# Performance work log

Measured on AMD Instinct MI355X. Metric: run time of the kernel, lower is better.

## Reference

```python
import jax, jax.numpy as jnp
import numpy as np

B, L = 1, 2048
HID, NH, VOCAB = 1024, 12, 50257
KD, VD = 768, 1536            # key_dim = 0.75*1024, value_dim = 1.5*1024
DK, DV = KD // NH, VD // NH   # 64, 128
CONV_K = 4
EPS = 1e-5

def silu(x):
    return x * jax.nn.sigmoid(x)

def short_conv(x, w):
    # causal depthwise conv1d: x [B,T,D], w [D,K]; y[t] = sum_i w[:,i]*x[t-(K-1)+i]
    T = x.shape[1]
    K = w.shape[1]
    xp = jnp.pad(x, ((0, 0), (K - 1, 0), (0, 0)))
    y = xp[:, 0:T, :] * w[:, 0]
    for i in range(1, K):
        y = y + xp[:, i:i + T, :] * w[:, i]
    return y

def l2norm(x):
    return x * jax.lax.rsqrt(jnp.sum(x * x, -1, keepdims=True) + 1e-6)

def setup_inputs() -> dict:
    key = jax.random.key(0)
    ks = jax.random.split(key, 16)
    n = lambda k, shape, s: jax.random.normal(k, shape, jnp.float32) * s
    dt = jnp.exp(jax.random.uniform(ks[12], (NH,)) * (np.log(0.1) - np.log(0.001)) + np.log(0.001))
    dt = jnp.clip(dt, 1e-4, None)
    return {
        "hidden_states": jax.random.randint(ks[0], (B, L), 0, VOCAB),
        "emb": n(ks[1], (VOCAB, HID), 0.02),
        "Wq": n(ks[2], (KD, HID), 0.02),
        "Wk": n(ks[3], (KD, HID), 0.02),
        "Wv": n(ks[4], (VD, HID), 0.02),
        "Wg": n(ks[5], (VD, HID), 0.02),
        "wq_conv": n(ks[6], (KD, CONV_K), 0.3),
        "wk_conv": n(ks[7], (KD, CONV_K), 0.3),
        "wv_conv": n(ks[8], (VD, CONV_K), 0.3),
        "Wgk": n(ks[9], (NH, HID), 0.02),
        "Wb": n(ks[10], (NH, HID), 0.02),
        "b_b": jnp.zeros((NH,), jnp.float32),
        "A_log": jnp.log(jax.random.uniform(ks[11], (NH,), minval=1.0, maxval=16.0)),
        "dt_bias": dt + jnp.log(-jnp.expm1(-dt)),
        "g_norm_w": jnp.ones((DV,), jnp.float32),
        "Wo": n(ks[13], (HID, VD), 0.02),
        "Wlm": n(ks[14], (VOCAB, HID), 0.02),
        "b_lm": jnp.zeros((VOCAB,), jnp.float32),
    }

def reference(hidden_states, emb, Wq, Wk, Wv, Wg, wq_conv, wk_conv, wv_conv,
              Wgk, Wb, b_b, A_log, dt_bias, g_norm_w, Wo, Wlm, b_lm):
    x = emb[hidden_states]                                   # [B,L,HID]
    q = silu(short_conv(x @ Wq.T, wq_conv))                  # [B,L,KD]
    k = silu(short_conv(x @ Wk.T, wk_conv))                  # [B,L,KD]
    v = silu(short_conv(x @ Wv.T, wv_conv))                  # [B,L,VD]
    # mamba-style per-head log-decay gate
    gk = -jnp.exp(A_log) * jax.nn.softplus(x @ Wgk.T + dt_bias)  # [B,L,NH]
    beta = jax.nn.sigmoid(x @ Wb.T + b_b)                        # [B,L,NH]
    q = l2norm(q.reshape(B, L, NH, DK)) * (DK ** -0.5)
    k = l2norm(k.reshape(B, L, NH, DK))
    v = v.reshape(B, L, NH, DV)
    # time-major for the gated delta-rule recurrence
    qs = q.transpose(1, 0, 2, 3)
    ks_ = k.transpose(1, 0, 2, 3)
    vs = v.transpose(1, 0, 2, 3)
    gks = gk.transpose(1, 0, 2)
    bs = beta.transpose(1, 0, 2)
    S0 = jnp.zeros((B, NH, DK, DV), jnp.float32)

    def step(S, inp):
        q_t, k_t, v_t, g_t, b_t = inp                        # [B,NH,DK],[B,NH,DK],[B,NH,DV],[B,NH],[B,NH]
        S = S * jnp.exp(g_t)[..., None, None]                # per-head scalar decay
        v_old = jnp.einsum('bhk,bhkv->bhv', k_t, S)
        dv = (v_t - v_old) * b_t[..., None]                  # delta-rule correction
        S = S + k_t[..., None] * dv[:, :, None, :]           # rank-1 update
        o_t = jnp.einsum('bhk,bhkv->bhv', q_t, S)
        return S, o_t

    _, o = jax.lax.scan(step, S0, (qs, ks_, vs, gks, bs))    # [L,B,NH,DV]
    o = o.transpose(1, 0, 2, 3)                              # [B,L,NH,DV]
    g = (x @ Wg.T).reshape(B, L, NH, DV)
    # fused RMSNorm + swish gate: rmsnorm(o) * g * sigmoid(g)
    o = o * jax.lax.rsqrt(jnp.mean(o * o, -1, keepdims=True) + EPS) * g_norm_w
    o = o * silu(g)
    o = o.reshape(B, L, VD) @ Wo.T                           # [B,L,HID]
    return o @ Wlm.T + b_lm                                  # [B,L,VOCAB]
```

## Files before the change

kernel.cpp:

```cpp
#include <hip/hip_runtime.h>
#include <math.h>

typedef float fx4 __attribute__((ext_vector_type(4)));
typedef _Float16 hx8 __attribute__((ext_vector_type(8)));
typedef _Float16 hx4 __attribute__((ext_vector_type(4)));

#define GL16(g, l) __builtin_amdgcn_global_load_lds( \
    (const __attribute__((address_space(1))) void*)(g), \
    (__attribute__((address_space(3))) void*)(l), 16, 0, 0)

template<bool NTL>
__global__ __launch_bounds__(256)
void cvt16(const float* __restrict__ in, _Float16* __restrict__ outh, int n8)
{
  int i = blockIdx.x * 256 + threadIdx.x;
  if (i < n8){
    fx4 a, b;
    if (NTL){
      a = __builtin_nontemporal_load((const fx4*)(in + (size_t)i * 8));
      b = __builtin_nontemporal_load((const fx4*)(in + (size_t)i * 8 + 4));
    } else {
      a = *(const fx4*)(in + (size_t)i * 8);
      b = *(const fx4*)(in + (size_t)i * 8 + 4);
    }
    hx8 h;
    #pragma unroll
    for (int e = 0; e < 4; e++){ h[e] = (_Float16)a[e]; h[4+e] = (_Float16)b[e]; }
    *(hx8*)(outh + (size_t)i * 8) = h;
  }
}

__global__ __launch_bounds__(256)
void embed_k(const int* __restrict__ ids, const float* __restrict__ emb,
             float* __restrict__ x, _Float16* __restrict__ xh)
{
  int t = blockIdx.x;
  int id = ids[t];
  fx4 v = *(const fx4*)(emb + (size_t)id * 1024 + threadIdx.x * 4);
  *(fx4*)(x + (size_t)t * 1024 + threadIdx.x * 4) = v;
  hx4 h;
  #pragma unroll
  for (int e = 0; e < 4; e++) h[e] = (_Float16)v[e];
  *(hx4*)(xh + (size_t)t * 1024 + threadIdx.x * 4) = h;
}

template<int MT, int NT, int WR, int WC, bool OUT16>
__global__ __launch_bounds__(WR*WC*64, 2)
void gemm_hh(const _Float16* __restrict__ A, const _Float16* __restrict__ B,
             void* __restrict__ Cv, const float* __restrict__ bias,
             int M, int N, int K)
{
  constexpr int BM = WR*MT*16, BN = WC*NT*16;
  constexpr int T  = WR*WC*64;
  constexpr int ABYTES = BM*128, BUF = ABYTES + BN*128;
  constexpr int FA = BM*8/T, FB = BN*8/T;
  static_assert(FA + FB == 4, "vmcnt literal assumes 4 loads/thread/tile");
  __shared__ __align__(16) char smem[2*BUF];

  const int tid = threadIdx.x;
  const int lane = tid & 63, w = tid >> 6;
  const int wr = w / WC, wc = w % WC;
  const int lm = lane & 15, lg = lane >> 4;
  const int nk = K >> 6;

  const int nwgx = gridDim.x, nwg = nwgx * gridDim.y;
  int orig = blockIdx.y * nwgx + blockIdx.x;
  int logical = (orig & 7) * (nwg >> 3) + (orig >> 3);
  const int m0 = (logical % nwgx) * BM, n0 = (logical / nwgx) * BN;

  const char* gsA[FA];
  const char* gsB[FB];
  int fdA[FA], fdB[FB];
  #pragma unroll
  for (int j = 0; j < FA; j++){
    int f = tid + j*T;
    int row = f >> 3, oct = (f & 7) ^ (row & 7);
    gsA[j] = (const char*)(A + (size_t)(m0 + row) * K + oct * 8);
    fdA[j] = f * 16;
  }
  #pragma unroll
  for (int j = 0; j < FB; j++){
    int f = tid + j*T;
    int row = f >> 3, oct = (f & 7) ^ (row & 7);
    int rb = n0 + row; if (rb > N - 1) rb = N - 1;
    gsB[j] = (const char*)(B + (size_t)rb * K + oct * 8);
    fdB[j] = ABYTES + f * 16;
  }

  fx4 acc[MT][NT];
  #pragma unroll
  for (int mt = 0; mt < MT; mt++)
    #pragma unroll
    for (int nt = 0; nt < NT; nt++)
      acc[mt][nt] = (fx4){0.f, 0.f, 0.f, 0.f};

  #pragma unroll
  for (int j = 0; j < FA; j++) GL16(gsA[j], smem + fdA[j]);
  #pragma unroll
  for (int j = 0; j < FB; j++) GL16(gsB[j], smem + fdB[j]);
  if (nk > 1){
    #pragma unroll
    for (int j = 0; j < FA; j++) GL16(gsA[j] + 128, smem + BUF + fdA[j]);
    #pragma unroll
    for (int j = 0; j < FB; j++) GL16(gsB[j] + 128, smem + BUF + fdB[j]);
  }

  for (int kt = 0; kt < nk; kt++){
    if (kt + 1 < nk) asm volatile("s_waitcnt vmcnt(4)" ::: "memory");
    else             asm volatile("s_waitcnt vmcnt(0)" ::: "memory");
    asm volatile("s_barrier" ::: "memory");

    const char* bp = smem + (kt & 1) * BUF;
    #pragma unroll
    for (int s = 0; s < 2; s++){
      hx8 af[MT], bfr[NT];
      #pragma unroll
      for (int mt = 0; mt < MT; mt++){
        int row = wr*MT*16 + mt*16 + lm;
        af[mt] = *(const hx8*)(bp + row*128 + (((s*4 + lg) ^ (row & 7)) << 4));
      }
      #pragma unroll
      for (int nt = 0; nt < NT; nt++){
        int row = wc*NT*16 + nt*16 + lm;
        bfr[nt] = *(const hx8*)(bp + ABYTES + row*128 + (((s*4 + lg) ^ (row & 7)) << 4));
      }
      #pragma unroll
      for (int mt = 0; mt < MT; mt++)
        #pragma unroll
        for (int nt = 0; nt < NT; nt++)
          acc[mt][nt] = __builtin_amdgcn_mfma_f32_16x16x32_f16(af[mt], bfr[nt], acc[mt][nt], 0, 0, 0);
    }
    asm volatile("s_barrier" ::: "memory");

    if (kt + 2 < nk){
      char* nb = smem + (kt & 1) * BUF;
      size_t ko = (size_t)(kt + 2) * 128;
      #pragma unroll
      for (int j = 0; j < FA; j++) GL16(gsA[j] + ko, nb + fdA[j]);
      #pragma unroll
      for (int j = 0; j < FB; j++) GL16(gsB[j] + ko, nb + fdB[j]);
    }
  }

  if (OUT16){
    _Float16* Ch = (_Float16*)Cv;
    #pragma unroll
    for (int nt = 0; nt < NT; nt++){
      int col = n0 + wc*NT*16 + nt*16 + lm;
      if (col < N){
        #pragma unroll
        for (int mt = 0; mt < MT; mt++){
          int r0 = m0 + wr*MT*16 + mt*16 + (lg << 2);
          #pragma unroll
          for (int j = 0; j < 4; j++)
            Ch[(size_t)(r0 + j) * N + col] = (_Float16)acc[mt][nt][j];
        }
      }
    }
  } else {
    float* C = (float*)Cv;
    #pragma unroll
    for (int nt = 0; nt < NT; nt++){
      int col = n0 + wc*NT*16 + nt*16 + lm;
      if (col < N){
        float bsv = bias ? bias[col] : 0.f;
        #pragma unroll
        for (int mt = 0; mt < MT; mt++){
          int r0 = m0 + wr*MT*16 + mt*16 + (lg << 2);
          #pragma unroll
          for (int j = 0; j < 4; j++)
            C[(size_t)(r0 + j) * N + col] = acc[mt][nt][j] + bsv;
        }
      }
    }
  }
}

__global__ __launch_bounds__(256)
void gkbeta_f(const float* __restrict__ x, const float* __restrict__ Wgk,
              const float* __restrict__ Wb, const float* __restrict__ b_b,
              const float* __restrict__ A_log, const float* __restrict__ dtb,
              float* __restrict__ gko, float* __restrict__ beto)
{
  int t = blockIdx.x, tid = threadIdx.x, lane = tid & 63, w = tid >> 6;
  __shared__ __align__(16) float xs[1024];
  __shared__ float res[24];
  *(fx4*)&xs[tid * 4] = *(const fx4*)(x + (size_t)t * 1024 + tid * 4);
  __syncthreads();
  for (int r = w; r < 24; r += 4){
    const float* wrow = (r < 12) ? (Wgk + r * 1024) : (Wb + (r - 12) * 1024);
    float a = 0.f;
    #pragma unroll
    for (int j = 0; j < 16; j++) a += xs[lane + j * 64] * wrow[lane + j * 64];
    #pragma unroll
    for (int d = 1; d < 64; d <<= 1) a += __shfl_xor(a, d, 64);
    if (lane == 0) res[r] = a;
  }
  __syncthreads();
  if (tid < 12){
    float z = res[tid] + dtb[tid];
    float sp = (z > 20.f) ? z : log1pf(expf(z));
    gko [(size_t)t * 12 + tid] = -expf(A_log[tid]) * sp;
    float b = res[12 + tid] + b_b[tid];
    beto[(size_t)t * 12 + tid] = 1.f / (1.f + expf(-b));
  }
}

__global__ __launch_bounds__(256)
void conv_fused(const float* __restrict__ qkvg, const float* __restrict__ wqc,
                const float* __restrict__ wkc, const float* __restrict__ wvc,
                float* __restrict__ qpp, float* __restrict__ kpp,
                float* __restrict__ vpp)
{
  int traw = blockIdx.x;
  int t = (traw & 7) * 256 + (traw >> 3);
  int gc = blockIdx.y * 256 + threadIdx.x;
  const float* cw; int cc;
  if (gc < 768){ cw = wqc; cc = gc; }
  else if (gc < 1536){ cw = wkc; cc = gc - 768; }
  else { cw = wvc; cc = gc - 1536; }
  float y = 0.f;
  #pragma unroll
  for (int i = 0; i < 4; i++){
    int ts = t - 3 + i;
    if (ts >= 0) y += cw[cc * 4 + i] * qkvg[(size_t)ts * 4608 + gc];
  }
  y = y / (1.f + expf(-y));
  if (gc < 1536){
    float ss = y * y;
    #pragma unroll
    for (int d = 1; d < 64; d <<= 1) ss += __shfl_xor(ss, d, 64);
    y *= rsqrtf(ss + 1e-6f) * (gc < 768 ? 0.125f : 1.0f);
  }
  if (gc < 768)       qpp[(size_t)t * 768 + gc] = y;
  else if (gc < 1536) kpp[(size_t)t * 768 + gc - 768] = y;
  else                vpp[(size_t)t * 1536 + gc - 1536] = y;
}

__global__ __launch_bounds__(256)
void phaseA(const float* __restrict__ qp, const float* __restrict__ kp,
            const float* __restrict__ vp, const float* __restrict__ gkv,
            const float* __restrict__ bev, float* __restrict__ Wt,
            float* __restrict__ Uvv, float* __restrict__ Mg,
            float* __restrict__ Ng, float* __restrict__ Ca,
            float* __restrict__ bv)
{
  const int braw = blockIdx.x;
  const int blk = (braw & 7) * 48 + (braw >> 3);
  const int h = blk % 12, c = blk / 12, t0 = c * 64;
  const int tid = threadIdx.x;

  __shared__ __align__(16) float Kc[4096];
  __shared__ __align__(16) float X[12288];
  __shared__ float Pp[2016];
  __shared__ float gt[64], bb[64], be[64], eg[64];
  __shared__ float Gtot;

  {
    int i = tid >> 2, q4 = tid & 3;
    const float* src = kp + (size_t)(t0 + i) * 768 + h * 64 + q4 * 16;
    #pragma unroll
    for (int e = 0; e < 4; e++)
      *(fx4*)&Kc[i * 64 + q4 * 16 + e * 4] = *(const fx4*)(src + e * 4);
  }
  if (tid < 64){
    float g = gkv[(size_t)(t0 + tid) * 12 + h];
    #pragma unroll
    for (int d = 1; d < 64; d <<= 1){
      float ts = __shfl_up(g, d, 64);
      if (tid >= d) g += ts;
    }
    gt[tid] = g;
    bb[tid] = expf(g);
    be[tid] = bev[(size_t)(t0 + tid) * 12 + h];
    if (tid == 63) Gtot = g;
  }
  __syncthreads();
  const float GT = Gtot;
  if (tid < 64) eg[tid] = expf(GT - gt[tid]);

  {
    int i = tid >> 2, jb = tid & 3;
    float ki[64];
    #pragma unroll
    for (int d = 0; d < 64; d++) ki[d] = Kc[i * 64 + d];
    float gi = gt[i], bei = be[i];
    int pbase = (i * (i - 1)) >> 1;
    for (int jj = 0; jj < 16; jj++){
      int j = jb * 16 + jj;
      if (j < i){
        float dot = 0.f;
        #pragma unroll
        for (int d = 0; d < 64; d++) dot += ki[d] * Kc[j * 64 + d];
        Pp[pbase + j] = bei * dot * expf(gi - gt[j]);
      }
    }
  }
  {
    int i = tid >> 2, seg = tid & 3;
    float bei = be[i], bbi = bb[i];
    #pragma unroll
    for (int u = 0; u < 12; u++){
      int colv = seg * 48 + u * 4;
      fx4 val;
      if (colv < 128){
        val = *(const fx4*)(vp + (size_t)(t0 + i) * 1536 + h * 128 + colv);
        #pragma unroll
        for (int e = 0; e < 4; e++) val[e] *= bei;
      } else {
        int d0 = colv - 128;
        #pragma unroll
        for (int e = 0; e < 4; e++) val[e] = bei * bbi * Kc[i * 64 + d0 + e];
      }
      *(fx4*)&X[i * 192 + colv] = val;
    }
  }
  __syncthreads();

  for (int i = 1; i < 64; i++){
    if (tid < 192){
      int pbase = (i * (i - 1)) >> 1;
      float accv = 0.f;
      for (int j = 0; j < i; j++) accv += Pp[pbase + j] * X[j * 192 + tid];
      X[i * 192 + tid] -= accv;
    }
    __syncthreads();
  }

  for (int e = tid; e < 12288; e += 256){
    int i = e / 192, colv = e - i * 192;
    float xv = X[e];
    if (colv < 128) Uvv[(size_t)blk * 8192 + i * 128 + colv] = xv;
    else            Wt [(size_t)blk * 4096 + i * 64 + (colv - 128)] = xv;
  }

  {
    int d2 = tid & 63, d1b = tid >> 6;
    for (int ii = 0; ii < 16; ii++){
      int d1 = d1b * 16 + ii;
      float s = 0.f;
      for (int j = 0; j < 64; j++)
        s += eg[j] * Kc[j * 64 + d1] * X[j * 192 + 128 + d2];
      Mg[(size_t)blk * 4096 + d1 * 64 + d2] = ((d1 == d2) ? expf(GT) : 0.f) - s;
    }
  }
  {
    int vv = tid & 127, d1b = tid >> 7;
    for (int ii = 0; ii < 32; ii++){
      int d1 = d1b * 32 + ii;
      float s = 0.f;
      for (int j = 0; j < 64; j++)
        s += eg[j] * Kc[j * 64 + d1] * X[j * 192 + vv];
      Ng[(size_t)blk * 8192 + d1 * 128 + vv] = s;
    }
  }
  {
    int i = tid >> 2, jb = tid & 3;
    float qi[64];
    {
      const float* src = qp + (size_t)(t0 + i) * 768 + h * 64;
      #pragma unroll
      for (int q4 = 0; q4 < 16; q4++){
        fx4 t4 = *(const fx4*)(src + q4 * 4);
        #pragma unroll
        for (int e = 0; e < 4; e++) qi[q4 * 4 + e] = t4[e];
      }
    }
    float gi = gt[i];
    for (int jj = 0; jj < 16; jj++){
      int j = jb * 16 + jj;
      float outv = 0.f;
      if (j <= i){
        float dot = 0.f;
        #pragma unroll
        for (int d = 0; d < 64; d++) dot += qi[d] * Kc[j * 64 + d];
        outv = dot * expf(gi - gt[j]);
      }
      Ca[(size_t)blk * 4096 + i * 64 + j] = outv;
    }
  }
  if (tid < 64) bv[(size_t)blk * 64 + tid] = bb[tid];
}

__global__ __launch_bounds__(256)
void phaseB(const float* __restrict__ Mg, const float* __restrict__ Ng,
            float* __restrict__ Sst)
{
  const int h = blockIdx.x >> 2, v0 = (blockIdx.x & 3) * 32;
  const int tid = threadIdx.x, lane = tid & 63, w = tid >> 6;
  const int lm = lane & 15, lg = lane >> 4;
  __shared__ __align__(16) float ST[2048];

  #pragma unroll
  for (int e = 0; e < 2; e++)
    *(fx4*)&ST[(tid + e * 256) * 4] = (fx4){0.f,0.f,0.f,0.f};
  {
    float* dst = Sst + (size_t)h * 8192;
    #pragma unroll
    for (int e = 0; e < 2; e++){
      int r = (tid >> 3) + e * 32;
      *(fx4*)(dst + (size_t)r * 128 + v0 + (tid & 7) * 4) = (fx4){0.f,0.f,0.f,0.f};
    }
  }
  __syncthreads();

  fx4 rm[2][2];
  float rn[2][4];
  auto loadMN = [&](int cc){
    const float* mb = Mg + ((size_t)cc * 12 + h) * 4096 + (w * 16 + lm) * 64 + lg * 8;
    rm[0][0] = *(const fx4*)(mb);
    rm[0][1] = *(const fx4*)(mb + 4);
    rm[1][0] = *(const fx4*)(mb + 32);
    rm[1][1] = *(const fx4*)(mb + 36);
    const float* nb = Ng + ((size_t)cc * 12 + h) * 8192 + v0;
    #pragma unroll
    for (int nt = 0; nt < 2; nt++)
      #pragma unroll
      for (int j = 0; j < 4; j++)
        rn[nt][j] = nb[(w * 16 + lg * 4 + j) * 128 + nt * 16 + lm];
  };
  loadMN(0);

  for (int c = 0; c < 32; c++){
    hx8 mf[2];
    #pragma unroll
    for (int s = 0; s < 2; s++)
      #pragma unroll
      for (int e = 0; e < 4; e++){
        mf[s][e]     = (_Float16)rm[s][0][e];
        mf[s][4 + e] = (_Float16)rm[s][1][e];
      }
    fx4 acc[2];
    #pragma unroll
    for (int nt = 0; nt < 2; nt++)
      #pragma unroll
      for (int j = 0; j < 4; j++) acc[nt][j] = rn[nt][j];
    if (c + 1 < 32) loadMN(c + 1);

    hx8 bfr[2][2];
    #pragma unroll
    for (int s = 0; s < 2; s++)
      #pragma unroll
      for (int nt = 0; nt < 2; nt++){
        int vv = nt * 16 + lm, kb = s * 4 + lg;
        fx4 p0 = *(const fx4*)&ST[kb * 256 + vv * 8];
        fx4 p1 = *(const fx4*)&ST[kb * 256 + vv * 8 + 4];
        #pragma unroll
        for (int e = 0; e < 4; e++){
          bfr[s][nt][e]     = (_Float16)p0[e];
          bfr[s][nt][4 + e] = (_Float16)p1[e];
        }
      }
    #pragma unroll
    for (int s = 0; s < 2; s++)
      #pragma unroll
      for (int nt = 0; nt < 2; nt++)
        acc[nt] = __builtin_amdgcn_mfma_f32_16x16x32_f16(mf[s], bfr[s][nt], acc[nt], 0, 0, 0);
    __syncthreads();
    float* dstS = (c + 1 < 32) ? (Sst + ((size_t)(c + 1) * 12 + h) * 8192 + v0) : nullptr;
    #pragma unroll
    for (int nt = 0; nt < 2; nt++){
      int vv = nt * 16 + lm;
      #pragma unroll
      for (int j = 0; j < 4; j++){
        int r = w * 16 + lg * 4 + j;
        ST[(r >> 3) * 256 + vv * 8 + (r & 7)] = acc[nt][j];
        if (dstS) dstS[(size_t)r * 128 + vv] = acc[nt][j];
      }
    }
    __syncthreads();
  }
}

__global__ __launch_bounds__(256)
void phaseC(const float* __restrict__ qp, const float* __restrict__ Sst,
            const float* __restrict__ Wt, const float* __restrict__ Uvv,
            const float* __restrict__ Ca, const float* __restrict__ bv,
            float* __restrict__ oraw)
{
  const int braw = blockIdx.x;
  const int blk = (braw & 7) * 48 + (braw >> 3);
  const int h = blk % 12, c = blk / 12, t0 = c * 64;
  const int tid = threadIdx.x;

  __shared__ __align__(16) float S0l[8192];
  __shared__ __align__(16) float Ul[8192];
  __shared__ __align__(16) float Wl[4096];
  __shared__ __align__(16) float Ql[4096];
  __shared__ float bl[64];

  #pragma unroll
  for (int e = 0; e < 8; e++){
    int i4 = tid + e * 256;
    *(fx4*)&S0l[i4 * 4] = *(const fx4*)(Sst + (size_t)blk * 8192 + i4 * 4);
    *(fx4*)&Ul[i4 * 4]  = *(const fx4*)(Uvv + (size_t)blk * 8192 + i4 * 4);
  }
  #pragma unroll
  for (int e = 0; e < 4; e++){
    int i4 = tid + e * 256;
    *(fx4*)&Wl[i4 * 4] = *(const fx4*)(Wt + (size_t)blk * 4096 + i4 * 4);
  }
  {
    int i = tid >> 2, q4 = tid & 3;
    const float* src = qp + (size_t)(t0 + i) * 768 + h * 64 + q4 * 16;
    #pragma unroll
    for (int e = 0; e < 4; e++)
      *(fx4*)&Ql[i * 64 + q4 * 16 + e * 4] = *(const fx4*)(src + e * 4);
  }
  if (tid < 64) bl[tid] = bv[(size_t)blk * 64 + tid];
  __syncthreads();

  const int v = tid & 127, rh = tid >> 7;
  float s0c[64];
  #pragma unroll
  for (int d = 0; d < 64; d++) s0c[d] = S0l[d * 128 + v];

  for (int j = rh * 32; j < rh * 32 + 32; j++){
    float accv = 0.f;
    #pragma unroll
    for (int d = 0; d < 64; d++) accv += Wl[j * 64 + d] * s0c[d];
    Ul[j * 128 + v] -= accv;
  }
  __syncthreads();
  #pragma unroll
  for (int e = 0; e < 4; e++){
    int i4 = tid + e * 256;
    *(fx4*)&Wl[i4 * 4] = *(const fx4*)(Ca + (size_t)blk * 4096 + i4 * 4);
  }
  __syncthreads();

  for (int i = rh * 32; i < rh * 32 + 32; i++){
    float aq = 0.f;
    #pragma unroll
    for (int d = 0; d < 64; d++) aq += Ql[i * 64 + d] * s0c[d];
    float ao = 0.f;
    for (int j = 0; j <= i; j++) ao += Wl[i * 64 + j] * Ul[j * 128 + v];
    oraw[(size_t)(t0 + i) * 1536 + h * 128 + v] = bl[i] * aq + ao;
  }
}

__global__ __launch_bounds__(256)
void rmsgate(const float* __restrict__ oraw, const float* __restrict__ gx,
             int gstride, const float* __restrict__ gnw, _Float16* __restrict__ ogh)
{
  int t = blockIdx.x, lane = threadIdx.x & 63;
  int h = blockIdx.y * 4 + (threadIdx.x >> 6);
  size_t base = (size_t)t * 1536 + h * 128;
  size_t gbase = (size_t)t * gstride + h * 128;
  float o1 = oraw[base + lane], o2 = oraw[base + 64 + lane];
  float ss = o1 * o1 + o2 * o2;
  #pragma unroll
  for (int d = 1; d < 64; d <<= 1) ss += __shfl_xor(ss, d, 64);
  float r = rsqrtf(ss * (1.f / 128.f) + 1e-5f);
  float g1 = gx[gbase + lane], g2 = gx[gbase + 64 + lane];
  ogh[base + lane]      = (_Float16)(o1 * r * gnw[lane]      * (g1 / (1.f + expf(-g1))));
  ogh[base + 64 + lane] = (_Float16)(o2 * r * gnw[64 + lane] * (g2 / (1.f + expf(-g2))));
}

extern "C" void kernel_launch(void* const* d_in, const int* in_sizes, int n_in,
                              void* d_out, int out_size, void* d_ws, size_t ws_size,
                              hipStream_t stream)
{
  const int*   ids   = (const int*)d_in[0];
  const float* emb   = (const float*)d_in[1];
  const float* Wq    = (const float*)d_in[2];
  const float* Wk    = (const float*)d_in[3];
  const float* Wv    = (const float*)d_in[4];
  const float* Wg    = (const float*)d_in[5];
  const float* wqc   = (const float*)d_in[6];
  const float* wkc   = (const float*)d_in[7];
  const float* wvc   = (const float*)d_in[8];
  const float* Wgk   = (const float*)d_in[9];
  const float* Wb    = (const float*)d_in[10];
  const float* b_b   = (const float*)d_in[11];
  const float* A_log = (const float*)d_in[12];
  const float* dtb   = (const float*)d_in[13];
  const float* gnw   = (const float*)d_in[14];
  const float* Wo    = (const float*)d_in[15];
  const float* Wlm   = (const float*)d_in[16];
  const float* b_lm  = (const float*)d_in[17];
  float* out = (float*)d_out;

  float* x    = out;
  float* qkvg = out + 2097152;
  float* qpp  = out + 11534336;
  float* kpp  = out + 13107200;
  float* vpp  = out + 14680064;
  float* gkb  = out + 17825792;
  float* bet  = out + 17850368;
  float* Wt   = out + 17874944;
  float* Uvv  = out + 19447808;
  float* Mg   = out + 22593536;
  float* Ng   = out + 24166400;
  float* Ca   = out + 27312128;
  float* bvv  = out + 28884992;
  float* Sst  = out + 28909568;
  float* oraw = out + 32055296;
  _Float16* x_h  = (_Float16*)(out + 35201024);
  _Float16* og_h = (_Float16*)(out + 36300000);

  _Float16* h_h     = (_Float16*)d_ws;
  _Float16* Wqkvg_h = h_h + 2097152;
  _Float16* Wo_h    = Wqkvg_h + 4718592;
  _Float16* Wlm_h   = Wo_h + 1572864;

  cvt16<false><<<384,  256, 0, stream>>>(Wq, Wqkvg_h,           98304);
  cvt16<false><<<384,  256, 0, stream>>>(Wk, Wqkvg_h +  786432, 98304);
  cvt16<false><<<768,  256, 0, stream>>>(Wv, Wqkvg_h + 1572864, 196608);
  cvt16<false><<<768,  256, 0, stream>>>(Wg, Wqkvg_h + 3145728, 196608);
  cvt16<false><<<768,  256, 0, stream>>>(Wo, Wo_h, 196608);
  cvt16<true ><<<25129, 256, 0, stream>>>(Wlm, Wlm_h, 6432896);

  embed_k<<<2048, 256, 0, stream>>>(ids, emb, x, x_h);
  gemm_hh<4,2,2,4,false><<<dim3(16, 36), 512, 0, stream>>>(x_h, Wqkvg_h, qkvg, nullptr, 2048, 4608, 1024);
  gkbeta_f<<<2048, 256, 0, stream>>>(x, Wgk, Wb, b_b, A_log, dtb, gkb, bet);
  conv_fused<<<dim3(2048, 12), 256, 0, stream>>>(qkvg, wqc, wkc, wvc, qpp, kpp, vpp);
  phaseA<<<384, 256, 0, stream>>>(qpp, kpp, vpp, gkb, bet, Wt, Uvv, Mg, Ng, Ca, bvv);
  phaseB<<<48, 256, 0, stream>>>(Mg, Ng, Sst);
  phaseC<<<384, 256, 0, stream>>>(qpp, Sst, Wt, Uvv, Ca, bvv, oraw);
  rmsgate<<<dim3(2048, 3), 256, 0, stream>>>(oraw, qkvg + 3072, 4608, gnw, og_h);
  gemm_hh<4,2,2,4,true><<<dim3(16, 8), 512, 0, stream>>>(og_h, Wo_h, h_h, nullptr, 2048, 1024, 1536);
  gemm_hh<4,2,2,4,false><<<dim3(16, 393), 512, 0, stream>>>(h_h, Wlm_h, out, b_lm, 2048, 50257, 1024);
}
```

Baseline: 843.5 us.

## Split K across wave groups in GEMM with LDS reduction of partial accumulators

Replaces the templated GEMM with a fixed 128x128 tile kernel where the eight waves form two groups, each handling one 32-wide half of every 64-wide K slice. Each wave now computes a 64x64 sub-tile (4x4 MFMAs) instead of 64x32, which raises the MFMA-to-LDS-read ratio per wave. Partial sums are combined through LDS at the end, with the second group writing and the first group adding and storing. This costs an extra reduction pass and leaves half the waves idle during the epilogue, and register pressure per wave roughly doubles for the accumulators.

```diff
diff --git a/kernel.cpp b/kernel.cpp
--- a/kernel.cpp
+++ b/kernel.cpp
@@ -44,65 +44,57 @@
   *(hx4*)(xh + (size_t)t * 1024 + threadIdx.x * 4) = h;
 }
 
-template<int MT, int NT, int WR, int WC, bool OUT16>
-__global__ __launch_bounds__(WR*WC*64, 2)
-void gemm_hh(const _Float16* __restrict__ A, const _Float16* __restrict__ B,
+template<bool OUT16>
+__global__ __launch_bounds__(512, 2)
+void gemm_ks(const _Float16* __restrict__ A, const _Float16* __restrict__ B,
              void* __restrict__ Cv, const float* __restrict__ bias,
              int M, int N, int K)
 {
-  constexpr int BM = WR*MT*16, BN = WC*NT*16;
-  constexpr int T  = WR*WC*64;
-  constexpr int ABYTES = BM*128, BUF = ABYTES + BN*128;
-  constexpr int FA = BM*8/T, FB = BN*8/T;
-  static_assert(FA + FB == 4, "vmcnt literal assumes 4 loads/thread/tile");
+  constexpr int ABYTES = 128*128, BUF = 2*ABYTES;
   __shared__ __align__(16) char smem[2*BUF];
 
   const int tid = threadIdx.x;
   const int lane = tid & 63, w = tid >> 6;
-  const int wr = w / WC, wc = w % WC;
+  const int s = w >> 2;
+  const int wr = (w >> 1) & 1, wc = w & 1;
   const int lm = lane & 15, lg = lane >> 4;
   const int nk = K >> 6;
 
   const int nwgx = gridDim.x, nwg = nwgx * gridDim.y;
   int orig = blockIdx.y * nwgx + blockIdx.x;
   int logical = (orig & 7) * (nwg >> 3) + (orig >> 3);
-  const int m0 = (logical % nwgx) * BM, n0 = (logical / nwgx) * BN;
-
-  const char* gsA[FA];
-  const char* gsB[FB];
-  int fdA[FA], fdB[FB];
-  #pragma unroll
-  for (int j = 0; j < FA; j++){
-    int f = tid + j*T;
+  const int m0 = (logical % nwgx) * 128, n0 = (logical / nwgx) * 128;
+
+  const char* gsA[2];
+  const char* gsB[2];
+  int fdA[2], fdB[2];
+  #pragma unroll
+  for (int j = 0; j < 2; j++){
+    int f = tid + j*512;
     int row = f >> 3, oct = (f & 7) ^ (row & 7);
     gsA[j] = (const char*)(A + (size_t)(m0 + row) * K + oct * 8);
     fdA[j] = f * 16;
-  }
-  #pragma unroll
-  for (int j = 0; j < FB; j++){
-    int f = tid + j*T;
-    int row = f >> 3, oct = (f & 7) ^ (row & 7);
     int rb = n0 + row; if (rb > N - 1) rb = N - 1;
     gsB[j] = (const char*)(B + (size_t)rb * K + oct * 8);
     fdB[j] = ABYTES + f * 16;
   }
 
-  fx4 acc[MT][NT];
-  #pragma unroll
-  for (int mt = 0; mt < MT; mt++)
-    #pragma unroll
-    for (int nt = 0; nt < NT; nt++)
+  fx4 acc[4][4];
+  #pragma unroll
+  for (int mt = 0; mt < 4; mt++)
+    #pragma unroll
+    for (int nt = 0; nt < 4; nt++)
       acc[mt][nt] = (fx4){0.f, 0.f, 0.f, 0.f};
 
   #pragma unroll
-  for (int j = 0; j < FA; j++) GL16(gsA[j], smem + fdA[j]);
-  #pragma unroll
-  for (int j = 0; j < FB; j++) GL16(gsB[j], smem + fdB[j]);
+  for (int j = 0; j < 2; j++){ GL16(gsA[j], smem + fdA[j]); }
+  #pragma unroll
+  for (int j = 0; j < 2; j++){ GL16(gsB[j], smem + fdB[j]); }
   if (nk > 1){
     #pragma unroll
-    for (int j = 0; j < FA; j++) GL16(gsA[j] + 128, smem + BUF + fdA[j]);
-    #pragma unroll
-    for (int j = 0; j < FB; j++) GL16(gsB[j] + 128, smem + BUF + fdB[j]);
+    for (int j = 0; j < 2; j++){ GL16(gsA[j] + 128, smem + BUF + fdA[j]); }
+    #pragma unroll
+    for (int j = 0; j < 2; j++){ GL16(gsB[j] + 128, smem + BUF + fdB[j]); }
   }
 
   for (int kt = 0; kt < nk; kt++){
@@ -111,65 +103,83 @@
     asm volatile("s_barrier" ::: "memory");
 
     const char* bp = smem + (kt & 1) * BUF;
-    #pragma unroll
-    for (int s = 0; s < 2; s++){
-      hx8 af[MT], bfr[NT];
-      #pragma unroll
-      for (int mt = 0; mt < MT; mt++){
-        int row = wr*MT*16 + mt*16 + lm;
-        af[mt] = *(const hx8*)(bp + row*128 + (((s*4 + lg) ^ (row & 7)) << 4));
-      }
-      #pragma unroll
-      for (int nt = 0; nt < NT; nt++){
-        int row = wc*NT*16 + nt*16 + lm;
-        bfr[nt] = *(const hx8*)(bp + ABYTES + row*128 + (((s*4 + lg) ^ (row & 7)) << 4));
-      }
-      #pragma unroll
-      for (int mt = 0; mt < MT; mt++)
-        #pragma unroll
-        for (int nt = 0; nt < NT; nt++)
-          acc[mt][nt] = __builtin_amdgcn_mfma_f32_16x16x32_f16(af[mt], bfr[nt], acc[mt][nt], 0, 0, 0);
-    }
+    hx8 af[4], bfr[4];
+    #pragma unroll
+    for (int mt = 0; mt < 4; mt++){
+      int row = wr*64 + mt*16 + lm;
+      af[mt] = *(const hx8*)(bp + row*128 + (((s*4 + lg) ^ (row & 7)) << 4));
+    }
+    #pragma unroll
+    for (int nt = 0; nt < 4; nt++){
+      int row = wc*64 + nt*16 + lm;
+      bfr[nt] = *(const hx8*)(bp + ABYTES + row*128 + (((s*4 + lg) ^ (row & 7)) << 4));
+    }
+    #pragma unroll
+    for (int mt = 0; mt < 4; mt++)
+      #pragma unroll
+      for (int nt = 0; nt < 4; nt++)
+        acc[mt][nt] = __builtin_amdgcn_mfma_f32_16x16x32_f16(af[mt], bfr[nt], acc[mt][nt], 0, 0, 0);
     asm volatile("s_barrier" ::: "memory");
 
     if (kt + 2 < nk){
       char* nb = smem + (kt & 1) * BUF;
       size_t ko = (size_t)(kt + 2) * 128;
       #pragma unroll
-      for (int j = 0; j < FA; j++) GL16(gsA[j] + ko, nb + fdA[j]);
-      #pragma unroll
-      for (int j = 0; j < FB; j++) GL16(gsB[j] + ko, nb + fdB[j]);
-    }
-  }
-
-  if (OUT16){
-    _Float16* Ch = (_Float16*)Cv;
-    #pragma unroll
-    for (int nt = 0; nt < NT; nt++){
-      int col = n0 + wc*NT*16 + nt*16 + lm;
-      if (col < N){
+      for (int j = 0; j < 2; j++){ GL16(gsA[j] + ko, nb + fdA[j]); }
+      #pragma unroll
+      for (int j = 0; j < 2; j++){ GL16(gsB[j] + ko, nb + fdB[j]); }
+    }
+  }
+
+  __syncthreads();
+  float* red = (float*)smem;
+  const int q = (w & 3) * 64 + lane;
+  if (s == 1){
+    #pragma unroll
+    for (int mt = 0; mt < 4; mt++)
+      #pragma unroll
+      for (int nt = 0; nt < 4; nt++)
+        *(fx4*)&red[((mt*4 + nt) * 256 + q) * 4] = acc[mt][nt];
+  }
+  __syncthreads();
+  if (s == 0){
+    #pragma unroll
+    for (int mt = 0; mt < 4; mt++)
+      #pragma unroll
+      for (int nt = 0; nt < 4; nt++){
+        fx4 o = *(const fx4*)&red[((mt*4 + nt) * 256 + q) * 4];
         #pragma unroll
-        for (int mt = 0; mt < MT; mt++){
-          int r0 = m0 + wr*MT*16 + mt*16 + (lg << 2);
+        for (int j = 0; j < 4; j++) acc[mt][nt][j] += o[j];
+      }
+    if (OUT16){
+      _Float16* Ch = (_Float16*)Cv;
+      #pragma unroll
+      for (int nt = 0; nt < 4; nt++){
+        int col = n0 + wc*64 + nt*16 + lm;
+        if (col < N){
           #pragma unroll
-          for (int j = 0; j < 4; j++)
-            Ch[(size_t)(r0 + j) * N + col] = (_Float16)acc[mt][nt][j];
+          for (int mt = 0; mt < 4; mt++){
+            int r0 = m0 + wr*64 + mt*16 + (lg << 2);
+            #pragma unroll
+            for (int j = 0; j < 4; j++)
+              Ch[(size_t)(r0 + j) * N + col] = (_Float16)acc[mt][nt][j];
+          }
         }
       }
-    }
-  } else {
-    float* C = (float*)Cv;
-    #pragma unroll
-    for (int nt = 0; nt < NT; nt++){
-      int col = n0 + wc*NT*16 + nt*16 + lm;
-      if (col < N){
-        float bsv = bias ? bias[col] : 0.f;
-        #pragma unroll
-        for (int mt = 0; mt < MT; mt++){
-          int r0 = m0 + wr*MT*16 + mt*16 + (lg << 2);
+    } else {
+      float* C = (float*)Cv;
+      #pragma unroll
+      for (int nt = 0; nt < 4; nt++){
+        int col = n0 + wc*64 + nt*16 + lm;
+        if (col < N){
+          float bsv = bias ? bias[col] : 0.f;
           #pragma unroll
-          for (int j = 0; j < 4; j++)
-            C[(size_t)(r0 + j) * N + col] = acc[mt][nt][j] + bsv;
+          for (int mt = 0; mt < 4; mt++){
+            int r0 = m0 + wr*64 + mt*16 + (lg << 2);
+            #pragma unroll
+            for (int j = 0; j < 4; j++)
+              C[(size_t)(r0 + j) * N + col] = acc[mt][nt][j] + bsv;
+          }
         }
       }
     }
@@ -612,13 +622,13 @@
   cvt16<true ><<<25129, 256, 0, stream>>>(Wlm, Wlm_h, 6432896);
 
   embed_k<<<2048, 256, 0, stream>>>(ids, emb, x, x_h);
-  gemm_hh<4,2,2,4,false><<<dim3(16, 36), 512, 0, stream>>>(x_h, Wqkvg_h, qkvg, nullptr, 2048, 4608, 1024);
+  gemm_ks<false><<<dim3(16, 36), 512, 0, stream>>>(x_h, Wqkvg_h, qkvg, nullptr, 2048, 4608, 1024);
   gkbeta_f<<<2048, 256, 0, stream>>>(x, Wgk, Wb, b_b, A_log, dtb, gkb, bet);
   conv_fused<<<dim3(2048, 12), 256, 0, stream>>>(qkvg, wqc, wkc, wvc, qpp, kpp, vpp);
   phaseA<<<384, 256, 0, stream>>>(qpp, kpp, vpp, gkb, bet, Wt, Uvv, Mg, Ng, Ca, bvv);
   phaseB<<<48, 256, 0, stream>>>(Mg, Ng, Sst);
   phaseC<<<384, 256, 0, stream>>>(qpp, Sst, Wt, Uvv, Ca, bvv, oraw);
   rmsgate<<<dim3(2048, 3), 256, 0, stream>>>(oraw, qkvg + 3072, 4608, gnw, og_h);
-  gemm_hh<4,2,2,4,true><<<dim3(16, 8), 512, 0, stream>>>(og_h, Wo_h, h_h, nullptr, 2048, 1024, 1536);
-  gemm_hh<4,2,2,4,false><<<dim3(16, 393), 512, 0, stream>>>(h_h, Wlm_h, out, b_lm, 2048, 50257, 1024);
-}
+  gemm_ks<true><<<dim3(16, 8), 512, 0, stream>>>(og_h, Wo_h, h_h, nullptr, 2048, 1024, 1536);
+  gemm_ks<false><<<dim3(16, 393), 512, 0, stream>>>(h_h, Wlm_h, out, b_lm, 2048, 50257, 1024);
+}
```

Measured after the change: 952.4 us. 1.13x slower.
